# Kernel optimization log

Hardware: AMD Instinct MI355X
Metric: run time of the kernel (lower is better)

Reference implementation:

```python
import jax, jax.numpy as jnp
import numpy as np

EPS = 1e-5
NUM_HEADS = 8


def _ln(x, g, b):
    m = jnp.mean(x, axis=-1, keepdims=True)
    v = jnp.var(x, axis=-1, keepdims=True)
    return (x - m) * jax.lax.rsqrt(v + EPS) * g + b


def _adaptive_pool_mat(L, out):
    # torch F.adaptive_avg_pool1d bin edges: start=floor(i*L/out), end=ceil((i+1)*L/out)
    i = np.arange(out)
    start = (i * L) // out
    end = -((-(i + 1) * L) // out)
    W = np.zeros((out, L), np.float32)
    for r in range(out):
        W[r, start[r]:end[r]] = 1.0 / (end[r] - start[r])
    return jnp.asarray(W)


def _sparse_mask(S, key):
    # True = blocked. Local band of width ~0.1*S plus random unblocked entries per row.
    keep = max(1, int(S * 0.1))
    half = keep // 2
    idx = jnp.arange(S)
    band = (idx[None, :] >= idx[:, None] - half) & (idx[None, :] <= idx[:, None] + half)
    blocked = ~band
    if keep > 4:
        num_random = max(1, keep // 4)
        keys = jax.random.split(key, S)
        rand_idx = jax.vmap(lambda k: jax.random.permutation(k, S)[:num_random])(keys)
        blocked = blocked.at[idx[:, None], rand_idx].set(False)
    return blocked


def setup_inputs() -> dict:
    key = jax.random.key(0)
    ks = jax.random.split(key, 12)
    B, C, H, W = 1, 256, 64, 64
    s = lambda k, shp: jax.random.normal(k, shp, jnp.float32) * 0.02
    return dict(
        x=jax.random.normal(ks[0], (B, C, H, W), jnp.float32),
        local_pos=s(ks[1], (1, C)),
        reg_pos0=s(ks[2], (1, C)),
        reg_pos1=s(ks[3], (1, C)),
        ln_local_g=jnp.ones((C,), jnp.float32), ln_local_b=jnp.zeros((C,), jnp.float32),
        ln_reg0_g=jnp.ones((C,), jnp.float32), ln_reg0_b=jnp.zeros((C,), jnp.float32),
        ln_reg1_g=jnp.ones((C,), jnp.float32), ln_reg1_b=jnp.zeros((C,), jnp.float32),
        adj0_w=s(ks[4], (C, C * 16)), adj0_b=jnp.zeros((C,), jnp.float32),
        adj1_w=s(ks[5], (C, C * 64)), adj1_b=jnp.zeros((C,), jnp.float32),
        in_proj_w=s(ks[6], (3 * C, C)), in_proj_b=jnp.zeros((3 * C,), jnp.float32),
        out_w=s(ks[7], (C, C)), out_b=jnp.zeros((C,), jnp.float32),
        ln_out_g=jnp.ones((C,), jnp.float32), ln_out_b=jnp.zeros((C,), jnp.float32),
        mlp_w1=s(ks[8], (4 * C, C)), mlp_b1=jnp.zeros((4 * C,), jnp.float32),
        mlp_w2=s(ks[9], (C, 4 * C)), mlp_b2=jnp.zeros((C,), jnp.float32),
    )


def reference(x, local_pos, reg_pos0, reg_pos1,
              ln_local_g, ln_local_b, ln_reg0_g, ln_reg0_b, ln_reg1_g, ln_reg1_b,
              adj0_w, adj0_b, adj1_w, adj1_b,
              in_proj_w, in_proj_b, out_w, out_b,
              ln_out_g, ln_out_b, mlp_w1, mlp_b1, mlp_w2, mlp_b2):
    B, C, H, W = x.shape
    HW = H * W
    # local branch: [B, HW, C]
    x_flat = x.reshape(B, C, HW).transpose(0, 2, 1)
    local_f = _ln(x_flat + local_pos[0], ln_local_g, ln_local_b)
    # regional branches (patch sizes 4, 8): each produces C tokens of dim C
    regional = []
    for ps, rp, lg, lb, aw, ab in ((4, reg_pos0, ln_reg0_g, ln_reg0_b, adj0_w, adj0_b),
                                   (8, reg_pos1, ln_reg1_g, ln_reg1_b, adj1_w, adj1_b)):
        N = (H // ps) * (W // ps)
        xp = x.reshape(B, C, H // ps, ps, W // ps, ps)
        xp = xp.transpose(0, 2, 4, 1, 3, 5).reshape(B, N, C * ps * ps)
        pool = _adaptive_pool_mat(N, C)          # [C, N] pools token dim N -> C
        xp = jnp.einsum('bnd,cn->bcd', xp, pool)  # [B, C, C*ps*ps]
        xp = xp @ aw.T + ab                        # dim_adjust -> [B, C, C]
        regional.append(_ln(xp + rp[0], lg, lb))
    feats = jnp.concatenate([local_f] + regional, axis=1)  # [B, S, C]
    S = feats.shape[1]
    blocked = _sparse_mask(S, jax.random.key(42))
    # MultiheadAttention (eval, dropout off)
    dh = C // NUM_HEADS
    qkv = feats @ in_proj_w.T + in_proj_b
    q, k, v = jnp.split(qkv, 3, axis=-1)
    heads = lambda t: t.reshape(B, S, NUM_HEADS, dh).transpose(0, 2, 1, 3)
    q, k, v = heads(q), heads(k), heads(v)
    scores = jnp.einsum('bhqd,bhkd->bhqk', q, k) / jnp.sqrt(jnp.float32(dh))
    scores = jnp.where(blocked, -jnp.inf, scores)
    attn = jax.nn.softmax(scores, axis=-1)
    ctx = jnp.einsum('bhqk,bhkd->bhqd', attn, v).transpose(0, 2, 1, 3).reshape(B, S, C)
    attn_out = ctx @ out_w.T + out_b
    # take local tokens, residual MLP, fold back to image, outer residual
    lo = attn_out[:, :HW]
    h1 = jax.nn.gelu(_ln(lo, ln_out_g, ln_out_b) @ mlp_w1.T + mlp_b1, approximate=False)
    lo = lo + (h1 @ mlp_w2.T + mlp_b2)
    return lo.transpose(0, 2, 1).reshape(B, C, H, W) + x
```

## Files before the change

### kernel.cpp

```cpp
#include <hip/hip_runtime.h>
#include <hip/hip_bf16.h>
#include <cstdint>

#define THREEFRY_PARTITIONABLE 1

#define C_DIM 256
#define HW 4096
#define S_TOK 4608
#define NRAND 115
#define NW 144
#define HALF_BAND 230
#define CANDCAP 208
#define PTP 40
#define NHEADS 8

#define NB_MASK 4096
#define NB_TR   1024
#define NB_ADJ1 128
#define NB_ADJ2 128

typedef __attribute__((ext_vector_type(8))) short bf16x8;
typedef __attribute__((ext_vector_type(4))) float f32x4;
typedef __attribute__((ext_vector_type(16))) float f32x16;

__device__ __forceinline__ bool isbf(const void* gref) {
  return *(const uint32_t*)gref != 0x3F800000u;
}
__device__ __forceinline__ float ldin(const void* p, int i, bool bf) {
  if (bf) return __bfloat162float(((const __hip_bfloat16*)p)[i]);
  return ((const float*)p)[i];
}
__device__ __forceinline__ void stout(void* p, int i, float v, bool bf) {
  if (bf) ((__hip_bfloat16*)p)[i] = __float2bfloat16(v);
  else ((float*)p)[i] = v;
}
__device__ __forceinline__ uint16_t f2bf(float f) {
  __hip_bfloat16 h = __float2bfloat16(f);
  return *(uint16_t*)&h;
}
__device__ __forceinline__ float bfu2f(uint32_t u16) {
  return __uint_as_float(u16 << 16);
}
__device__ __forceinline__ void ld4f(const void* X, bool bf, int idx, float* o) {
  if (bf) {
    const ushort4 u = *(const ushort4*)((const uint16_t*)X + idx);
    o[0] = bfu2f(u.x); o[1] = bfu2f(u.y); o[2] = bfu2f(u.z); o[3] = bfu2f(u.w);
  } else {
    const float4 f = *(const float4*)((const float*)X + idx);
    o[0] = f.x; o[1] = f.y; o[2] = f.z; o[3] = f.w;
  }
}

__device__ __forceinline__ void tf2x32(uint32_t k0, uint32_t k1,
                                       uint32_t x0, uint32_t x1,
                                       uint32_t& o0, uint32_t& o1) {
  const uint32_t k2 = k0 ^ k1 ^ 0x1BD11BDAu;
  x0 += k0; x1 += k1;
#define TFR(r) x0 += x1; x1 = (x1 << (r)) | (x1 >> (32 - (r))); x1 ^= x0;
  TFR(13) TFR(15) TFR(26) TFR(6)
  x0 += k1; x1 += k2 + 1u;
  TFR(17) TFR(29) TFR(16) TFR(24)
  x0 += k2; x1 += k0 + 2u;
  TFR(13) TFR(15) TFR(26) TFR(6)
  x0 += k0; x1 += k1 + 3u;
  TFR(17) TFR(29) TFR(16) TFR(24)
  x0 += k1; x1 += k2 + 4u;
  TFR(13) TFR(15) TFR(26) TFR(6)
  x0 += k2; x1 += k0 + 5u;
#undef TFR
  o0 = x0; o1 = x1;
}

__device__ __forceinline__ float blockSum256(float v, float* rb, int tid) {
#pragma unroll
  for (int o = 32; o > 0; o >>= 1) v += __shfl_down(v, o, 64);
  if ((tid & 63) == 0) rb[tid >> 6] = v;
  __syncthreads();
  float r = rb[0] + rb[1] + rb[2] + rb[3];
  __syncthreads();
  return r;
}

#define LDP 40

template <int MODE>
__device__ __forceinline__ void adj_body(const void* X, const void* Bmat, float* Cout,
                                         int N, int K, int bn, int bm, int k0base,
                                         uint16_t* As, uint16_t* Bs, bool bf, int tid) {
  const int wave = tid >> 6, lane = tid & 63;
  const int l15 = lane & 15, quad = lane >> 4;
  const int srow = tid >> 2, scg = tid & 3;
  f32x4 acc[4] = {{0.f, 0.f, 0.f, 0.f}, {0.f, 0.f, 0.f, 0.f}, {0.f, 0.f, 0.f, 0.f}, {0.f, 0.f, 0.f, 0.f}};

  for (int k0 = k0base; k0 < k0base + 512; k0 += 32) {
    {
      const int m = bm + srow;
      const int d0 = k0 + scg * 8;
      float av[8];
      if (MODE == 1) {
        const int hr = m >> 4, wr = m & 15;
        const int cch = d0 >> 4;
        const int i0 = (d0 >> 2) & 3;
        ld4f(X, bf, cch * HW + (hr * 4 + i0) * 64 + wr * 4, av);
        ld4f(X, bf, cch * HW + (hr * 4 + i0 + 1) * 64 + wr * 4, av + 4);
      } else {
        const int hr = m >> 3, wr = m & 7;
        const int cch = d0 >> 6, ii = (d0 >> 3) & 7;
        const int base = cch * HW + (hr * 8 + ii) * 64 + wr * 8;
        ld4f(X, bf, base, av);
        ld4f(X, bf, base + 4, av + 4);
      }
      uint4 w;
      w.x = (uint32_t)f2bf(av[0]) | ((uint32_t)f2bf(av[1]) << 16);
      w.y = (uint32_t)f2bf(av[2]) | ((uint32_t)f2bf(av[3]) << 16);
      w.z = (uint32_t)f2bf(av[4]) | ((uint32_t)f2bf(av[5]) << 16);
      w.w = (uint32_t)f2bf(av[6]) | ((uint32_t)f2bf(av[7]) << 16);
      *(uint4*)&As[srow * LDP + scg * 8] = w;
    }
    {
      const size_t boff = (size_t)(bn + srow) * K + k0 + scg * 8;
      uint4 w;
      if (bf) {
        w = *(const uint4*)((const uint16_t*)Bmat + boff);
      } else {
        const float* bp = (const float*)Bmat + boff;
        const float4 b0 = *(const float4*)bp;
        const float4 b1 = *(const float4*)(bp + 4);
        w.x = (uint32_t)f2bf(b0.x) | ((uint32_t)f2bf(b0.y) << 16);
        w.y = (uint32_t)f2bf(b0.z) | ((uint32_t)f2bf(b0.w) << 16);
        w.z = (uint32_t)f2bf(b1.x) | ((uint32_t)f2bf(b1.y) << 16);
        w.w = (uint32_t)f2bf(b1.z) | ((uint32_t)f2bf(b1.w) << 16);
      }
      *(uint4*)&Bs[srow * LDP + scg * 8] = w;
    }
    __syncthreads();
    const bf16x8 afrag = *(const bf16x8*)&As[(wave * 16 + l15) * LDP + quad * 8];
#pragma unroll
    for (int j = 0; j < 4; ++j) {
      const bf16x8 bfrag = *(const bf16x8*)&Bs[(j * 16 + l15) * LDP + quad * 8];
      acc[j] = __builtin_amdgcn_mfma_f32_16x16x32_bf16(afrag, bfrag, acc[j], 0, 0, 0);
    }
    __syncthreads();
  }
#pragma unroll
  for (int j = 0; j < 4; ++j) {
    const int n = bn + j * 16 + l15;
#pragma unroll
    for (int r = 0; r < 4; ++r) {
      const int m = bm + wave * 16 + quad * 4 + r;
      atomicAdd(&Cout[(size_t)m * N + n], acc[j][r]);
    }
  }
}

__global__ __launch_bounds__(512, 8) void k_pre(uint16_t* __restrict__ randl,
                                                const void* __restrict__ x, float* __restrict__ xt,
                                                const void* __restrict__ adj0_w, const void* __restrict__ adj1_w,
                                                float* __restrict__ yraw, const void* __restrict__ gref) {
  const int b = blockIdx.x;
  const int tid = threadIdx.x;
  __shared__ __align__(16) uint32_t keys1s[S_TOK];
  __shared__ uint16_t mem1[S_TOK];
  __shared__ uint8_t  b2hi[S_TOK];
  __shared__ uint32_t baseA[257];
  __shared__ uint32_t baseB[257];
  __shared__ uint32_t offs[256];
  __shared__ uint32_t candk[CANDCAP];
  __shared__ uint16_t candi[CANDCAP];
  __shared__ uint32_t posmask[NW];
  __shared__ uint8_t  hotb[256];
  __shared__ uint16_t randrow[128];
  __shared__ uint32_t wsum[8];
  __shared__ int ncand, Tsh, nrcnt;

  if (b >= NB_MASK) {
    if (tid >= 256) return;
    const bool bf = isbf(gref);
    if (b < NB_MASK + NB_TR) {
      float (*tile)[33] = (float(*)[33])keys1s;
      const int t = b - NB_MASK;
      const int n0 = (t & 127) * 32, c0 = (t >> 7) * 32;
      const int tx = tid & 31, ty = tid >> 5;
      for (int i = ty; i < 32; i += 8)
        tile[i][tx] = ldin(x, (c0 + i) * HW + n0 + tx, bf);
      __syncthreads();
      for (int i = ty; i < 32; i += 8)
        xt[(size_t)(n0 + i) * C_DIM + c0 + tx] = tile[tx][i];
      return;
    }
    uint16_t* As = (uint16_t*)keys1s;
    uint16_t* Bs = (uint16_t*)(keys1s + 1280);
    if (b < NB_MASK + NB_TR + NB_ADJ1) {
      const int t = b - (NB_MASK + NB_TR);
      adj_body<1>(x, adj0_w, yraw, 256, 4096,
                  (t & 3) * 64, ((t >> 2) & 3) * 64, (t >> 4) * 512, As, Bs, bf, tid);
    } else {
      const int t = b - (NB_MASK + NB_TR + NB_ADJ1);
      adj_body<2>(x, adj1_w, yraw + 256 * 256, 256, 16384,
                  (t & 3) * 64, 0, (t >> 2) * 512, As, Bs, bf, tid);
    }
    return;
  }

  const int q = b;
  uint32_t s10, s11, s20, s21;
  {
#if THREEFRY_PARTITIONABLE
    uint32_t kq0, kq1, ka0, ka1;
    tf2x32(0u, 42u, 0u, (uint32_t)q, kq0, kq1);
    tf2x32(kq0, kq1, 0u, 0u, ka0, ka1);
    tf2x32(kq0, kq1, 0u, 1u, s10, s11);
    tf2x32(ka0, ka1, 0u, 1u, s20, s21);
#else
    uint32_t o0, o1, k0, k1;
    uint32_t j = 2u * (uint32_t)q;
    if (j < S_TOK) { tf2x32(0u, 42u, j, j + S_TOK, o0, o1); k0 = o0; }
    else           { tf2x32(0u, 42u, j - S_TOK, j, o0, o1); k0 = o1; }
    j = 2u * (uint32_t)q + 1u;
    if (j < S_TOK) { tf2x32(0u, 42u, j, j + S_TOK, o0, o1); k1 = o0; }
    else           { tf2x32(0u, 42u, j - S_TOK, j, o0, o1); k1 = o1; }
    uint32_t a0, b0, a1, b1;
    tf2x32(k0, k1, 0u, 2u, a0, b0);
    tf2x32(k0, k1, 1u, 3u, a1, b1);
    s10 = b0; s11 = b1;
    uint32_t c0, d0, c1, d1;
    tf2x32(a0, a1, 0u, 2u, c0, d0);
    tf2x32(a0, a1, 1u, 3u, c1, d1);
    s20 = d0; s21 = d1;
#endif
  }
  if (tid == 0) { ncand = 0; Tsh = 0; nrcnt = 0; }
  if (tid < 256) { baseA[tid] = 0u; baseB[tid] = 0u; }
  for (int w = tid; w < NW; w += 512) posmask[w] = 0u;
  __syncthreads();

  uint32_t v1reg[9];
#pragma unroll
  for (int it = 0; it < 9; ++it) {
    const int i = tid + it * 512;
    uint32_t a, bb;
    tf2x32(s10, s11, 0u, (uint32_t)i, a, bb);
    const uint32_t v1 = a ^ bb;
    tf2x32(s20, s21, 0u, (uint32_t)i, a, bb);
    const uint32_t v2 = a ^ bb;
    v1reg[it] = v1;
    atomicAdd(&baseA[v1 >> 24], 1u);
    atomicAdd(&baseB[v2 >> 24], 1u);
    b2hi[i] = (uint8_t)(v2 >> 24);
  }
  __syncthreads();

  {
    const int g = tid >> 8;
    const int loc = tid & 255;
    uint32_t* base = g ? baseB : baseA;
    const uint32_t v = base[loc];
    uint32_t s = v;
    const int lane = tid & 63;
#pragma unroll
    for (int o = 1; o < 64; o <<= 1) {
      const uint32_t t = __shfl_up(s, o, 64);
      if (lane >= o) s += t;
    }
    if (lane == 63) wsum[g * 4 + (loc >> 6)] = s;
    __syncthreads();
    uint32_t woff = 0;
#pragma unroll
    for (int w = 0; w < 3; ++w)
      if (w < (loc >> 6)) woff += wsum[g * 4 + w];
    const uint32_t ex = woff + s - v;
    base[loc] = ex;
    if (loc == 255) base[256] = ex + v;
    if (g == 1 && (int)ex <= NRAND - 1) atomicMax(&Tsh, loc);
  }
  __syncthreads();
  if (tid < 256) offs[tid] = baseA[tid];
  const int T = Tsh;
  __syncthreads();

#pragma unroll
  for (int it = 0; it < 9; ++it) {
    const int i = tid + it * 512;
    const uint32_t v1 = v1reg[it];
    const uint32_t p = atomicAdd(&offs[v1 >> 24], 1u);
    keys1s[p] = v1;
    mem1[p] = (uint16_t)i;
    if ((int)b2hi[i] <= T) {
      uint32_t a, bb;
      tf2x32(s20, s21, 0u, (uint32_t)i, a, bb);
      const uint32_t v2 = a ^ bb;
      const int c = atomicAdd(&ncand, 1);
      if (c < CANDCAP) { candk[c] = v2; candi[c] = (uint16_t)i; }
    }
  }
  __syncthreads();

  const int nc = min(ncand, CANDCAP);
  for (int c = tid; c < nc; c += 512) {
    const uint32_t kk = candk[c];
    const uint16_t ii = candi[c];
    int r = 0;
    for (int c2 = 0; c2 < nc; ++c2) {
      const uint32_t k2 = candk[c2];
      if (k2 < kk || (k2 == kk && candi[c2] < ii)) ++r;
    }
    if (r < NRAND) atomicOr(&posmask[ii >> 5], 1u << (ii & 31));
  }
  __syncthreads();

  if (tid < 256) {
    const int s0 = (int)baseA[tid], e0 = (int)baseA[tid + 1];
    uint8_t hot = 0;
    if (s0 < e0) {
      for (int w = (s0 >> 5); w <= ((e0 - 1) >> 5); ++w) {
        const int lo = max(s0, w * 32) - w * 32;
        const int hi = min(e0 - 1, w * 32 + 31) - w * 32;
        const uint32_t range = ((hi == 31) ? 0xFFFFFFFFu : ((1u << (hi + 1)) - 1u)) & ~((1u << lo) - 1u);
        if (posmask[w] & range) { hot = 1; break; }
      }
    }
    hotb[tid] = hot;
  }
  __syncthreads();

  for (int p = tid; p < S_TOK; p += 512) {
    const uint32_t ke = keys1s[p];
    const uint32_t bk = ke >> 24;
    if (!hotb[bk]) continue;
    const int e = (int)mem1[p];
    const int s0 = (int)baseA[bk], e0 = (int)baseA[bk + 1];
    int less = 0, eq = 0;
    for (int m = s0; m < e0; ++m) {
      const uint32_t kf = keys1s[m];
      less += (int)(kf < ke);
      eq += (int)(kf == ke);
    }
    int R = s0 + less;
    if (eq > 1) {
      int r2 = 0;
      for (int m = s0; m < e0; ++m)
        if (keys1s[m] == ke && (int)mem1[m] < e) ++r2;
      R += r2;
    }
    if ((posmask[R >> 5] >> (R & 31)) & 1u) {
      const int c = atomicAdd(&nrcnt, 1);
      if (c < 128) randrow[c] = (uint16_t)e;
    }
  }
  __syncthreads();
  if (tid < NRAND) randl[(size_t)q * 128 + tid] = randrow[tid];
}

template <bool GELU, bool ADDSRC, bool OUTBF, bool SPLITK, bool ABF16>
__global__ __launch_bounds__(256) void k_gemm_mfma(const void* __restrict__ A, const void* __restrict__ B,
                                                   const void* __restrict__ bias, const float* __restrict__ SRC,
                                                   void* __restrict__ Cout, void* __restrict__ Cout2,
                                                   int M, int N, int K,
                                                   const void* __restrict__ gref) {
  const bool bf = isbf(gref);
  __shared__ uint16_t As[64 * LDP];
  __shared__ uint16_t Bs[64 * LDP];
  const int bn = blockIdx.x * 64, bm = blockIdx.y * 64;
  const int tid = threadIdx.x;
  const int wave = tid >> 6, lane = tid & 63;
  const int l15 = lane & 15, quad = lane >> 4;
  const int srow = tid >> 2, scg = tid & 3;
  int kBeg = 0, kEnd = K;
  bool lead = true;
  if (SPLITK) {
    const int Kc = K >> 1;
    kBeg = blockIdx.z * Kc; kEnd = kBeg + Kc;
    lead = (blockIdx.z == 0);
  }
  f32x4 acc[4] = {{0.f, 0.f, 0.f, 0.f}, {0.f, 0.f, 0.f, 0.f}, {0.f, 0.f, 0.f, 0.f}, {0.f, 0.f, 0.f, 0.f}};

  for (int k0 = kBeg; k0 < kEnd; k0 += 32) {
    {
      const size_t aoff = (size_t)(bm + srow) * K + k0 + scg * 8;
      uint4 w;
      if (ABF16) {
        w = *(const uint4*)((const uint16_t*)A + aoff);
      } else {
        const float* ap = (const float*)A + aoff;
        const float4 a0 = *(const float4*)ap;
        const float4 a1 = *(const float4*)(ap + 4);
        w.x = (uint32_t)f2bf(a0.x) | ((uint32_t)f2bf(a0.y) << 16);
        w.y = (uint32_t)f2bf(a0.z) | ((uint32_t)f2bf(a0.w) << 16);
        w.z = (uint32_t)f2bf(a1.x) | ((uint32_t)f2bf(a1.y) << 16);
        w.w = (uint32_t)f2bf(a1.z) | ((uint32_t)f2bf(a1.w) << 16);
      }
      *(uint4*)&As[srow * LDP + scg * 8] = w;
    }
    {
      const size_t boff = (size_t)(bn + srow) * K + k0 + scg * 8;
      uint4 w;
      if (bf) {
        w = *(const uint4*)((const uint16_t*)B + boff);
      } else {
        const float* bp = (const float*)B + boff;
        const float4 b0 = *(const float4*)bp;
        const float4 b1 = *(const float4*)(bp + 4);
        w.x = (uint32_t)f2bf(b0.x) | ((uint32_t)f2bf(b0.y) << 16);
        w.y = (uint32_t)f2bf(b0.z) | ((uint32_t)f2bf(b0.w) << 16);
        w.z = (uint32_t)f2bf(b1.x) | ((uint32_t)f2bf(b1.y) << 16);
        w.w = (uint32_t)f2bf(b1.z) | ((uint32_t)f2bf(b1.w) << 16);
      }
      *(uint4*)&Bs[srow * LDP + scg * 8] = w;
    }
    __syncthreads();
    const bf16x8 afrag = *(const bf16x8*)&As[(wave * 16 + l15) * LDP + quad * 8];
#pragma unroll
    for (int j = 0; j < 4; ++j) {
      const bf16x8 bfrag = *(const bf16x8*)&Bs[(j * 16 + l15) * LDP + quad * 8];
      acc[j] = __builtin_amdgcn_mfma_f32_16x16x32_bf16(afrag, bfrag, acc[j], 0, 0, 0);
    }
    __syncthreads();
  }
  void* outp = (SPLITK && blockIdx.z) ? Cout2 : Cout;
#pragma unroll
  for (int j = 0; j < 4; ++j) {
    const int n = bn + j * 16 + l15;
    const float bv = ldin(bias, n, bf);
#pragma unroll
    for (int r = 0; r < 4; ++r) {
      const int m = bm + wave * 16 + quad * 4 + r;
      float v = acc[j][r];
      if (lead) v += bv;
      if (GELU) v = 0.5f * v * (1.0f + erff(v * 0.70710678118654752f));
      if (ADDSRC && lead) v += SRC[(size_t)m * N + n];
      if (OUTBF) ((__hip_bfloat16*)outp)[(size_t)m * N + n] = __float2bfloat16(v);
      else ((float*)outp)[(size_t)m * N + n] = v;
    }
  }
}

__global__ __launch_bounds__(256) void k_ln(const float* __restrict__ X, const void* __restrict__ pos,
                                            const void* __restrict__ g, const void* __restrict__ b,
                                            __hip_bfloat16* __restrict__ Y, const void* __restrict__ gref) {
  const bool bf = isbf(gref);
  __shared__ float rb[4];
  const int row = blockIdx.x, c = threadIdx.x;
  float v = X[(size_t)row * C_DIM + c];
  if (pos) v += ldin(pos, c, bf);
  const float m = blockSum256(v, rb, c) * (1.f / 256.f);
  const float dd = v - m;
  const float var = blockSum256(dd * dd, rb, c) * (1.f / 256.f);
  Y[(size_t)row * C_DIM + c] = __float2bfloat16(dd * rsqrtf(var + 1e-5f) * ldin(g, c, bf) + ldin(b, c, bf));
}

__global__ __launch_bounds__(256) void k_ln_all(const float* __restrict__ xt,
                                                const float* __restrict__ y0, const float* __restrict__ y1,
                                                const void* lp, const void* rp0, const void* rp1,
                                                const void* gl, const void* bl,
                                                const void* g0, const void* b0,
                                                const void* g1, const void* b1,
                                                const void* ab0, const void* ab1,
                                                __hip_bfloat16* __restrict__ feats, const void* __restrict__ gref) {
  const bool bf = isbf(gref);
  __shared__ float rb[4];
  const int r = blockIdx.x, c = threadIdx.x;
  const float* src; const void *rp, *g, *bb, *ab;
  if (r < HW)            { src = xt + (size_t)r * C_DIM; rp = lp; g = gl; bb = bl; ab = nullptr; }
  else if (r < HW + 256) { src = y0 + (size_t)(r - HW) * C_DIM; rp = rp0; g = g0; bb = b0; ab = ab0; }
  else                   { src = y1 + (size_t)((r - HW - 256) >> 2) * C_DIM; rp = rp1; g = g1; bb = b1; ab = ab1; }
  float v = src[c] + ldin(rp, c, bf);
  if (ab) v += ldin(ab, c, bf);
  const float m = blockSum256(v, rb, c) * (1.f / 256.f);
  const float dd = v - m;
  const float var = blockSum256(dd * dd, rb, c) * (1.f / 256.f);
  feats[(size_t)r * C_DIM + c] = __float2bfloat16(dd * rsqrtf(var + 1e-5f) * ldin(g, c, bf) + ldin(bb, c, bf));
}

__global__ __launch_bounds__(256) void k_attn_mfma(const __hip_bfloat16* __restrict__ qkvb,
                                                   const uint16_t* __restrict__ randl,
                                                   __hip_bfloat16* __restrict__ ctx) {
  const int qt = blockIdx.x;
  const int h  = blockIdx.y;
  const int q0 = qt * 32;
  const int tid = threadIdx.x;
  const int w = tid >> 6, l = tid & 63;
  const int hh = l >> 5, col = l & 31;

  __shared__ float    qs[32][33];
  __shared__ __align__(16) uint16_t vt[4][32 * PTP];
  __shared__ __align__(16) uint16_t pt[4][32 * PTP];
  __shared__ float    rsc[32][116];
  __shared__ uint16_t rl[32][116];
  __shared__ float    denw[4][32];
  __shared__ float    denr[32];
  __shared__ float    ctxs[32][33];
  __shared__ int      nrr[32];

  const int lo_u = max(q0 - HALF_BAND, 0);
  const int hi_u = min(q0 + 31 + HALF_BAND, S_TOK - 1);
  const int nt = (hi_u - lo_u + 32) >> 5;

  if (tid < 32) { nrr[tid] = 0; denr[tid] = 0.f; }
  for (int e = tid; e < 1024; e += 256) {
    const int r = e >> 5, d = e & 31;
    qs[r][d] = __bfloat162float(qkvb[(size_t)(q0 + r) * 768 + h * 32 + d]);
    ctxs[r][d] = 0.f;
  }
  __syncthreads();
  {
    const int r = tid >> 3, g = tid & 7;
    const int q = q0 + r;
    const int lo_r = max(q - HALF_BAND, 0), hi_r = min(q + HALF_BAND, S_TOK - 1);
    for (int t = g; t < NRAND; t += 8) {
      const int k = (int)randl[(size_t)q * 128 + t];
      if (k < lo_r || k > hi_r) {
        const int c = atomicAdd(&nrr[r], 1);
        rl[r][c] = (uint16_t)k;
      }
    }
  }
  __syncthreads();

  const float scale = 0.17677669529663687f;
  const __hip_bfloat16* qrow = qkvb + (size_t)(q0 + col) * 768 + h * 32;
  const bf16x8 qa0 = *(const bf16x8*)(qrow + 8 * hh);
  const bf16x8 qa1 = *(const bf16x8*)(qrow + 16 + 8 * hh);

  f32x16 cacc = {0.f, 0.f, 0.f, 0.f, 0.f, 0.f, 0.f, 0.f, 0.f, 0.f, 0.f, 0.f, 0.f, 0.f, 0.f, 0.f};
  float dssum[16];
#pragma unroll
  for (int i = 0; i < 16; ++i) dssum[i] = 0.f;
  for (int kt = w; kt < nt; kt += 4) {
    const int kbase = lo_u + kt * 32;
    const __hip_bfloat16* krow = qkvb + (size_t)(kbase + col) * 768 + 256 + h * 32;
    const bf16x8 kb0 = *(const bf16x8*)(krow + 8 * hh);
    const bf16x8 kb1 = *(const bf16x8*)(krow + 16 + 8 * hh);
    const int key2 = l >> 1;
    const int dbase = (l & 1) * 16;
    const uint16_t* vsrc = (const uint16_t*)qkvb + (size_t)(kbase + key2) * 768 + 512 + h * 32 + dbase;
    uint32_t wv[8];
    *(uint4*)&wv[0] = *(const uint4*)vsrc;
    *(uint4*)&wv[4] = *(const uint4*)(vsrc + 8);
    f32x16 s = {0.f, 0.f, 0.f, 0.f, 0.f, 0.f, 0.f, 0.f, 0.f, 0.f, 0.f, 0.f, 0.f, 0.f, 0.f, 0.f};
    s = __builtin_amdgcn_mfma_f32_32x32x16_bf16(qa0, kb0, s, 0, 0, 0);
    s = __builtin_amdgcn_mfma_f32_32x32x16_bf16(qa1, kb1, s, 0, 0, 0);
    const int kk = kbase + col;
#pragma unroll
    for (int i = 0; i < 16; ++i) {
      const int qrl = (i & 3) + 8 * (i >> 2) + 4 * hh;
      const int qr = q0 + qrl;
      float e = 0.f;
      if (kk <= hi_u && kk >= qr - HALF_BAND && kk <= qr + HALF_BAND)
        e = __expf(s[i] * scale);
      dssum[i] += e;
      pt[w][qrl * PTP + col] = f2bf(e);
    }
#pragma unroll
    for (int j = 0; j < 8; ++j) {
      vt[w][(dbase + 2 * j) * PTP + key2] = (uint16_t)(wv[j] & 0xffffu);
      vt[w][(dbase + 2 * j + 1) * PTP + key2] = (uint16_t)(wv[j] >> 16);
    }
    asm volatile("s_waitcnt lgkmcnt(0)" ::: "memory");
#pragma unroll
    for (int g2 = 0; g2 < 2; ++g2) {
      const bf16x8 pa = *(const bf16x8*)&pt[w][col * PTP + 16 * g2 + 8 * hh];
      const bf16x8 vb = *(const bf16x8*)&vt[w][col * PTP + 16 * g2 + 8 * hh];
      cacc = __builtin_amdgcn_mfma_f32_32x32x16_bf16(pa, vb, cacc, 0, 0, 0);
    }
  }
#pragma unroll
  for (int o = 1; o < 32; o <<= 1)
#pragma unroll
    for (int i = 0; i < 16; ++i) dssum[i] += __shfl_xor(dssum[i], o, 64);
  if (col == 0)
#pragma unroll
    for (int i = 0; i < 16; ++i) denw[w][(i & 3) + 8 * (i >> 2) + 4 * hh] = dssum[i];
#pragma unroll
  for (int i = 0; i < 16; ++i)
    atomicAdd(&ctxs[(i & 3) + 8 * (i >> 2) + 4 * hh][col], cacc[i]);

  {
    const int r = tid >> 3, g = tid & 7;
    const int nr = nrr[r];
    float dsum = 0.f;
    for (int i = g; i < nr; i += 8) {
      const int k = (int)rl[r][i];
      const uint4* kp = (const uint4*)(qkvb + (size_t)k * 768 + 256 + h * 32);
      float ds2 = 0.f;
#pragma unroll
      for (int t = 0; t < 4; ++t) {
        const uint4 kw = kp[t];
        ds2 += qs[r][8 * t + 0] * bfu2f(kw.x & 0xffffu) + qs[r][8 * t + 1] * __uint_as_float(kw.x & 0xffff0000u);
        ds2 += qs[r][8 * t + 2] * bfu2f(kw.y & 0xffffu) + qs[r][8 * t + 3] * __uint_as_float(kw.y & 0xffff0000u);
        ds2 += qs[r][8 * t + 4] * bfu2f(kw.z & 0xffffu) + qs[r][8 * t + 5] * __uint_as_float(kw.z & 0xffff0000u);
        ds2 += qs[r][8 * t + 6] * bfu2f(kw.w & 0xffffu) + qs[r][8 * t + 7] * __uint_as_float(kw.w & 0xffff0000u);
      }
      const float e = __expf(ds2 * scale);
      rsc[r][i] = e;
      dsum += e;
    }
#pragma unroll
    for (int o = 1; o < 8; o <<= 1) dsum += __shfl_xor(dsum, o, 64);
    if (g == 0) denr[r] = dsum;
  }
  __syncthreads();
  {
    const int r = tid >> 3, g = tid & 7;
    const int nr = nrr[r];
    float r0 = 0.f, r1 = 0.f, r2 = 0.f, r3 = 0.f;
#pragma unroll 4
    for (int i = 0; i < nr; ++i) {
      const int k = (int)rl[r][i];
      const float e = rsc[r][i];
      const uint2 vw = *(const uint2*)(qkvb + (size_t)k * 768 + 512 + h * 32 + g * 4);
      r0 += e * bfu2f(vw.x & 0xffffu);
      r1 += e * __uint_as_float(vw.x & 0xffff0000u);
      r2 += e * bfu2f(vw.y & 0xffffu);
      r3 += e * __uint_as_float(vw.y & 0xffff0000u);
    }
    atomicAdd(&ctxs[r][g * 4 + 0], r0);
    atomicAdd(&ctxs[r][g * 4 + 1], r1);
    atomicAdd(&ctxs[r][g * 4 + 2], r2);
    atomicAdd(&ctxs[r][g * 4 + 3], r3);
  }
  __syncthreads();
  {
    const int r = tid >> 3, d0 = (tid & 7) * 4;
    const float den = fmaxf(denw[0][r] + denw[1][r] + denw[2][r] + denw[3][r] + denr[r], 1e-30f);
    const float inv = 1.f / den;
#pragma unroll
    for (int j = 0; j < 4; ++j)
      ctx[(size_t)(q0 + r) * C_DIM + h * 32 + d0 + j] = __float2bfloat16(ctxs[r][d0 + j] * inv);
  }
}

__global__ __launch_bounds__(256) void k_final(const float* __restrict__ lo2a, const float* __restrict__ lo2b,
                                               const void* __restrict__ x,
                                               void* __restrict__ out, const void* __restrict__ gref) {
  const bool bf = isbf(gref);
  __shared__ float tile[32][33];
  const int n0 = blockIdx.x * 32, c0 = blockIdx.y * 32;
  const int tx = threadIdx.x & 31, ty = threadIdx.x >> 5;
  for (int i = ty; i < 32; i += 8) {
    const size_t o = (size_t)(n0 + i) * C_DIM + c0 + tx;
    tile[i][tx] = lo2a[o] + lo2b[o];
  }
  __syncthreads();
  for (int i = ty; i < 32; i += 8) {
    const int o = (c0 + i) * HW + n0 + tx;
    stout(out, o, tile[tx][i] + ldin(x, o, bf), bf);
  }
}

extern "C" void kernel_launch(void* const* d_in, const int* in_sizes, int n_in,
                              void* d_out, int out_size, void* d_ws, size_t ws_size,
                              hipStream_t stream) {
  const void* x          = d_in[0];
  const void* local_pos  = d_in[1];
  const void* reg_pos0   = d_in[2];
  const void* reg_pos1   = d_in[3];
  const void* ln_local_g = d_in[4];
  const void* ln_local_b = d_in[5];
  const void* ln_reg0_g  = d_in[6];
  const void* ln_reg0_b  = d_in[7];
  const void* ln_reg1_g  = d_in[8];
  const void* ln_reg1_b  = d_in[9];
  const void* adj0_w     = d_in[10];
  const void* adj0_b     = d_in[11];
  const void* adj1_w     = d_in[12];
  const void* adj1_b     = d_in[13];
  const void* in_proj_w  = d_in[14];
  const void* in_proj_b  = d_in[15];
  const void* out_w      = d_in[16];
  const void* out_b      = d_in[17];
  const void* ln_out_g   = d_in[18];
  const void* ln_out_b   = d_in[19];
  const void* mlp_w1     = d_in[20];
  const void* mlp_b1     = d_in[21];
  const void* mlp_w2     = d_in[22];
  const void* mlp_b2     = d_in[23];
  char* ws = (char*)d_ws;

  float* xt      = (float*)(ws + 0);
  float* yraw    = (float*)(ws + 4194304);
  __hip_bfloat16* feats = (__hip_bfloat16*)(ws + 4718592);
  __hip_bfloat16* qkvb  = (__hip_bfloat16*)(ws + 9437184);
  uint16_t* randl = (uint16_t*)(ws + 23592960);
  __hip_bfloat16* ctx  = (__hip_bfloat16*)(ws + 0);
  float* lo      = (float*)(ws + 4194304);
  __hip_bfloat16* lnlo = (__hip_bfloat16*)(ws + 8388608);
  __hip_bfloat16* h1   = (__hip_bfloat16*)(ws + 12582912);
  float* lo2a    = (float*)(ws + 0);
  float* lo2b    = (float*)(ws + 8388608);

  const void* gref = ln_local_g;

  hipMemsetAsync(yraw, 0, 320 * 256 * sizeof(float), stream);
  k_pre<<<dim3(NB_MASK + NB_TR + NB_ADJ1 + NB_ADJ2), 512, 0, stream>>>(randl, x, xt, adj0_w, adj1_w, yraw, gref);
  k_ln_all<<<dim3(S_TOK), 256, 0, stream>>>(xt, yraw, yraw + 256 * 256,
                                            local_pos, reg_pos0, reg_pos1,
                                            ln_local_g, ln_local_b, ln_reg0_g, ln_reg0_b,
                                            ln_reg1_g, ln_reg1_b, adj0_b, adj1_b, feats, gref);
  k_gemm_mfma<false, false, true, false, true><<<dim3(12, 72), 256, 0, stream>>>(feats, in_proj_w, in_proj_b, nullptr, qkvb, nullptr, S_TOK, 768, 256, gref);
  k_attn_mfma<<<dim3(HW / 32, NHEADS), 256, 0, stream>>>(qkvb, randl, ctx);
  k_gemm_mfma<false, false, false, false, true><<<dim3(4, 64), 256, 0, stream>>>(ctx, out_w, out_b, nullptr, lo, nullptr, HW, 256, 256, gref);
  k_ln<<<dim3(HW), 256, 0, stream>>>(lo, nullptr, ln_out_g, ln_out_b, lnlo, gref);
  k_gemm_mfma<true, false, true, false, true><<<dim3(16, 64), 256, 0, stream>>>(lnlo, mlp_w1, mlp_b1, nullptr, h1, nullptr, HW, 1024, 256, gref);
  k_gemm_mfma<false, true, false, true, true><<<dim3(4, 64, 2), 256, 0, stream>>>(h1, mlp_w2, mlp_b2, lo, lo2a, lo2b, HW, 256, 1024, gref);
  k_final<<<dim3(HW / 32, C_DIM / 32), 256, 0, stream>>>(lo2a, lo2b, x, d_out, gref);
}
```

Baseline: 427.2 us.

## Keep attention probabilities in registers via transposed MFMA and split-K out-proj

The band-attention score MFMA now computes K·Q^T, so each lane holds a key-row slice. The exponentiated scores are packed to bf16 and exchanged across half-waves with shuffles to form the A operand of the PV MFMA, which removes the shared-memory staging buffer for probabilities and the 16-way per-row denominator reductions. Random-key scores are stored as bf16 in shared memory to shrink LDS use, trading a little precision. The out-projection GEMM is also split along K across two blocks, and the partial sums are combined in the LayerNorm and in the MLP residual epilogue to raise parallelism.

```diff
diff --git a/kernel.cpp b/kernel.cpp
--- a/kernel.cpp
+++ b/kernel.cpp
@@ -354,6 +354,7 @@
 template <bool GELU, bool ADDSRC, bool OUTBF, bool SPLITK, bool ABF16>
 __global__ __launch_bounds__(256) void k_gemm_mfma(const void* __restrict__ A, const void* __restrict__ B,
                                                    const void* __restrict__ bias, const float* __restrict__ SRC,
+                                                   const float* __restrict__ SRC2,
                                                    void* __restrict__ Cout, void* __restrict__ Cout2,
                                                    int M, int N, int K,
                                                    const void* __restrict__ gref) {
@@ -427,21 +428,24 @@
       float v = acc[j][r];
       if (lead) v += bv;
       if (GELU) v = 0.5f * v * (1.0f + erff(v * 0.70710678118654752f));
-      if (ADDSRC && lead) v += SRC[(size_t)m * N + n];
+      if (ADDSRC && lead) {
+        v += SRC[(size_t)m * N + n];
+        if (SRC2) v += SRC2[(size_t)m * N + n];
+      }
       if (OUTBF) ((__hip_bfloat16*)outp)[(size_t)m * N + n] = __float2bfloat16(v);
       else ((float*)outp)[(size_t)m * N + n] = v;
     }
   }
 }
 
-__global__ __launch_bounds__(256) void k_ln(const float* __restrict__ X, const void* __restrict__ pos,
+__global__ __launch_bounds__(256) void k_ln(const float* __restrict__ X, const float* __restrict__ X2,
                                             const void* __restrict__ g, const void* __restrict__ b,
                                             __hip_bfloat16* __restrict__ Y, const void* __restrict__ gref) {
   const bool bf = isbf(gref);
   __shared__ float rb[4];
   const int row = blockIdx.x, c = threadIdx.x;
   float v = X[(size_t)row * C_DIM + c];
-  if (pos) v += ldin(pos, c, bf);
+  if (X2) v += X2[(size_t)row * C_DIM + c];
   const float m = blockSum256(v, rb, c) * (1.f / 256.f);
   const float dd = v - m;
   const float var = blockSum256(dd * dd, rb, c) * (1.f / 256.f);
@@ -483,8 +487,7 @@
 
   __shared__ float    qs[32][33];
   __shared__ __align__(16) uint16_t vt[4][32 * PTP];
-  __shared__ __align__(16) uint16_t pt[4][32 * PTP];
-  __shared__ float    rsc[32][116];
+  __shared__ uint16_t rsc[32][116];
   __shared__ uint16_t rl[32][116];
   __shared__ float    denw[4][32];
   __shared__ float    denr[32];
@@ -518,18 +521,17 @@
 
   const float scale = 0.17677669529663687f;
   const __hip_bfloat16* qrow = qkvb + (size_t)(q0 + col) * 768 + h * 32;
-  const bf16x8 qa0 = *(const bf16x8*)(qrow + 8 * hh);
-  const bf16x8 qa1 = *(const bf16x8*)(qrow + 16 + 8 * hh);
+  const bf16x8 qb0 = *(const bf16x8*)(qrow + 8 * hh);
+  const bf16x8 qb1 = *(const bf16x8*)(qrow + 16 + 8 * hh);
+  const int qr = q0 + col;
 
   f32x16 cacc = {0.f, 0.f, 0.f, 0.f, 0.f, 0.f, 0.f, 0.f, 0.f, 0.f, 0.f, 0.f, 0.f, 0.f, 0.f, 0.f};
-  float dssum[16];
-#pragma unroll
-  for (int i = 0; i < 16; ++i) dssum[i] = 0.f;
+  float dsum_band = 0.f;
   for (int kt = w; kt < nt; kt += 4) {
     const int kbase = lo_u + kt * 32;
     const __hip_bfloat16* krow = qkvb + (size_t)(kbase + col) * 768 + 256 + h * 32;
-    const bf16x8 kb0 = *(const bf16x8*)(krow + 8 * hh);
-    const bf16x8 kb1 = *(const bf16x8*)(krow + 16 + 8 * hh);
+    const bf16x8 ka0 = *(const bf16x8*)(krow + 8 * hh);
+    const bf16x8 ka1 = *(const bf16x8*)(krow + 16 + 8 * hh);
     const int key2 = l >> 1;
     const int dbase = (l & 1) * 16;
     const uint16_t* vsrc = (const uint16_t*)qkvb + (size_t)(kbase + key2) * 768 + 512 + h * 32 + dbase;
@@ -537,39 +539,46 @@
     *(uint4*)&wv[0] = *(const uint4*)vsrc;
     *(uint4*)&wv[4] = *(const uint4*)(vsrc + 8);
     f32x16 s = {0.f, 0.f, 0.f, 0.f, 0.f, 0.f, 0.f, 0.f, 0.f, 0.f, 0.f, 0.f, 0.f, 0.f, 0.f, 0.f};
-    s = __builtin_amdgcn_mfma_f32_32x32x16_bf16(qa0, kb0, s, 0, 0, 0);
-    s = __builtin_amdgcn_mfma_f32_32x32x16_bf16(qa1, kb1, s, 0, 0, 0);
-    const int kk = kbase + col;
-#pragma unroll
-    for (int i = 0; i < 16; ++i) {
-      const int qrl = (i & 3) + 8 * (i >> 2) + 4 * hh;
-      const int qr = q0 + qrl;
-      float e = 0.f;
-      if (kk <= hi_u && kk >= qr - HALF_BAND && kk <= qr + HALF_BAND)
-        e = __expf(s[i] * scale);
-      dssum[i] += e;
-      pt[w][qrl * PTP + col] = f2bf(e);
-    }
+    s = __builtin_amdgcn_mfma_f32_32x32x16_bf16(ka0, qb0, s, 0, 0, 0);
+    s = __builtin_amdgcn_mfma_f32_32x32x16_bf16(ka1, qb1, s, 0, 0, 0);
 #pragma unroll
     for (int j = 0; j < 8; ++j) {
       vt[w][(dbase + 2 * j) * PTP + key2] = (uint16_t)(wv[j] & 0xffffu);
       vt[w][(dbase + 2 * j + 1) * PTP + key2] = (uint16_t)(wv[j] >> 16);
     }
+    float e[16];
+#pragma unroll
+    for (int i = 0; i < 16; ++i) {
+      const int kk = kbase + (i & 3) + 8 * (i >> 2) + 4 * hh;
+      float ev = 0.f;
+      if (kk <= hi_u && kk >= qr - HALF_BAND && kk <= qr + HALF_BAND)
+        ev = __expf(s[i] * scale);
+      e[i] = ev;
+      dsum_band += ev;
+    }
+    uint32_t wn[8], pn[8];
+#pragma unroll
+    for (int j = 0; j < 4; ++j) {
+      wn[2 * j]     = (uint32_t)f2bf(e[4 * j])     | ((uint32_t)f2bf(e[4 * j + 1]) << 16);
+      wn[2 * j + 1] = (uint32_t)f2bf(e[4 * j + 2]) | ((uint32_t)f2bf(e[4 * j + 3]) << 16);
+    }
+#pragma unroll
+    for (int j = 0; j < 8; ++j) pn[j] = (uint32_t)__shfl_xor((int)wn[j], 32, 64);
     asm volatile("s_waitcnt lgkmcnt(0)" ::: "memory");
 #pragma unroll
     for (int g2 = 0; g2 < 2; ++g2) {
-      const bf16x8 pa = *(const bf16x8*)&pt[w][col * PTP + 16 * g2 + 8 * hh];
+      uint4 pw;
+      pw.x = hh ? pn[4 * g2 + 2] : wn[4 * g2];
+      pw.y = hh ? pn[4 * g2 + 3] : wn[4 * g2 + 1];
+      pw.z = hh ? wn[4 * g2 + 2] : pn[4 * g2];
+      pw.w = hh ? wn[4 * g2 + 3] : pn[4 * g2 + 1];
+      const bf16x8 pa = *(const bf16x8*)&pw;
       const bf16x8 vb = *(const bf16x8*)&vt[w][col * PTP + 16 * g2 + 8 * hh];
       cacc = __builtin_amdgcn_mfma_f32_32x32x16_bf16(pa, vb, cacc, 0, 0, 0);
     }
   }
-#pragma unroll
-  for (int o = 1; o < 32; o <<= 1)
-#pragma unroll
-    for (int i = 0; i < 16; ++i) dssum[i] += __shfl_xor(dssum[i], o, 64);
-  if (col == 0)
-#pragma unroll
-    for (int i = 0; i < 16; ++i) denw[w][(i & 3) + 8 * (i >> 2) + 4 * hh] = dssum[i];
+  dsum_band += __shfl_xor(dsum_band, 32, 64);
+  if (l < 32) denw[w][col] = dsum_band;
 #pragma unroll
   for (int i = 0; i < 16; ++i)
     atomicAdd(&ctxs[(i & 3) + 8 * (i >> 2) + 4 * hh][col], cacc[i]);
@@ -591,7 +600,7 @@
         ds2 += qs[r][8 * t + 6] * bfu2f(kw.w & 0xffffu) + qs[r][8 * t + 7] * __uint_as_float(kw.w & 0xffff0000u);
       }
       const float e = __expf(ds2 * scale);
-      rsc[r][i] = e;
+      rsc[r][i] = f2bf(e);
       dsum += e;
     }
 #pragma unroll
@@ -606,7 +615,7 @@
 #pragma unroll 4
     for (int i = 0; i < nr; ++i) {
       const int k = (int)rl[r][i];
-      const float e = rsc[r][i];
+      const float e = bfu2f(rsc[r][i]);
       const uint2 vw = *(const uint2*)(qkvb + (size_t)k * 768 + 512 + h * 32 + g * 4);
       r0 += e * bfu2f(vw.x & 0xffffu);
       r1 += e * __uint_as_float(vw.x & 0xffff0000u);
@@ -682,7 +691,8 @@
   __hip_bfloat16* qkvb  = (__hip_bfloat16*)(ws + 9437184);
   uint16_t* randl = (uint16_t*)(ws + 23592960);
   __hip_bfloat16* ctx  = (__hip_bfloat16*)(ws + 0);
-  float* lo      = (float*)(ws + 4194304);
+  float* lo_a    = (float*)(ws + 4194304);
+  float* lo_b    = (float*)(ws + 23592960);
   __hip_bfloat16* lnlo = (__hip_bfloat16*)(ws + 8388608);
   __hip_bfloat16* h1   = (__hip_bfloat16*)(ws + 12582912);
   float* lo2a    = (float*)(ws + 0);
@@ -696,11 +706,11 @@
                                             local_pos, reg_pos0, reg_pos1,
                                             ln_local_g, ln_local_b, ln_reg0_g, ln_reg0_b,
                                             ln_reg1_g, ln_reg1_b, adj0_b, adj1_b, feats, gref);
-  k_gemm_mfma<false, false, true, false, true><<<dim3(12, 72), 256, 0, stream>>>(feats, in_proj_w, in_proj_b, nullptr, qkvb, nullptr, S_TOK, 768, 256, gref);
+  k_gemm_mfma<false, false, true, false, true><<<dim3(12, 72), 256, 0, stream>>>(feats, in_proj_w, in_proj_b, nullptr, nullptr, qkvb, nullptr, S_TOK, 768, 256, gref);
   k_attn_mfma<<<dim3(HW / 32, NHEADS), 256, 0, stream>>>(qkvb, randl, ctx);
-  k_gemm_mfma<false, false, false, false, true><<<dim3(4, 64), 256, 0, stream>>>(ctx, out_w, out_b, nullptr, lo, nullptr, HW, 256, 256, gref);
-  k_ln<<<dim3(HW), 256, 0, stream>>>(lo, nullptr, ln_out_g, ln_out_b, lnlo, gref);
-  k_gemm_mfma<true, false, true, false, true><<<dim3(16, 64), 256, 0, stream>>>(lnlo, mlp_w1, mlp_b1, nullptr, h1, nullptr, HW, 1024, 256, gref);
-  k_gemm_mfma<false, true, false, true, true><<<dim3(4, 64, 2), 256, 0, stream>>>(h1, mlp_w2, mlp_b2, lo, lo2a, lo2b, HW, 256, 1024, gref);
+  k_gemm_mfma<false, false, false, true, true><<<dim3(4, 64, 2), 256, 0, stream>>>(ctx, out_w, out_b, nullptr, nullptr, lo_a, lo_b, HW, 256, 256, gref);
+  k_ln<<<dim3(HW), 256, 0, stream>>>(lo_a, lo_b, ln_out_g, ln_out_b, lnlo, gref);
+  k_gemm_mfma<true, false, true, false, true><<<dim3(16, 64), 256, 0, stream>>>(lnlo, mlp_w1, mlp_b1, nullptr, nullptr, h1, nullptr, HW, 1024, 256, gref);
+  k_gemm_mfma<false, true, false, true, true><<<dim3(4, 64, 2), 256, 0, stream>>>(h1, mlp_w2, mlp_b2, lo_a, lo_b, lo2a, lo2b, HW, 256, 1024, gref);
   k_final<<<dim3(HW / 32, C_DIM / 32), 256, 0, stream>>>(lo2a, lo2b, x, d_out, gref);
 }
```

Measured after the change: 417.1 us. -2.4%, faster.
